# Performance work log

Hardware: AMD Instinct MI355X
Metric: run time of the kernel (lower is better)

The kernel has to match this reference:

```python
import jax, jax.numpy as jnp
import numpy as np

NUM_CLASSES = 80
SCORE_THRESH = 0.5
NMS_THRESH = 0.5
TOP_K = 200  # max candidates kept per (image, class) before greedy NMS


def setup_inputs() -> dict:
    key = jax.random.key(0)
    k1, k2, k3 = jax.random.split(key, 3)
    B, A, HW, C = 8, 3, 5776, NUM_CLASSES  # 608-input YOLOv4 P3 level: 76*76
    # well-formed boxes in [0,1]: x1y1 + positive wh
    xy = jax.random.uniform(k1, (B, A, HW, 2)) * 0.8
    wh = jax.random.uniform(k2, (B, A, HW, 2)) * 0.2 + 0.01
    boxes = jnp.concatenate([xy, xy + wh], axis=-1)
    scores = jax.random.uniform(k3, (B, A, HW, C))
    return {"boxes": boxes, "scores": scores}


def _pairwise_iou(b):
    # b: [K, 4] (x1, y1, x2, y2) -> IoU matrix [K, K] (union mode)
    x1, y1, x2, y2 = b[:, 0], b[:, 1], b[:, 2], b[:, 3]
    area = (x2 - x1) * (y2 - y1)
    xx1 = jnp.maximum(x1[:, None], x1[None, :])
    yy1 = jnp.maximum(y1[:, None], y1[None, :])
    xx2 = jnp.minimum(x2[:, None], x2[None, :])
    yy2 = jnp.minimum(y2[:, None], y2[None, :])
    inter = jnp.maximum(0.0, xx2 - xx1) * jnp.maximum(0.0, yy2 - yy1)
    return inter / (area[:, None] + area[None, :] - inter)


def _nms_one(boxes, scores):
    # boxes: [N, 4], scores: [N] -> top-K candidates with greedy-NMS keep mask
    s = jnp.where(scores > SCORE_THRESH, scores, -jnp.inf)  # score threshold filter
    top_s, idx = jax.lax.top_k(s, TOP_K)                    # descending, like argsort()[::-1]
    b = boxes[idx]                                          # [K, 4]
    valid = jnp.isfinite(top_s)
    iou = _pairwise_iou(b)                                  # [K, K]

    def body(keep, i):
        # if box i survives, suppress all lower-scored boxes with IoU > thresh
        sup = keep[i] & (iou[i] > NMS_THRESH) & (jnp.arange(TOP_K) > i)
        return keep & ~sup, None

    keep, _ = jax.lax.scan(body, valid, jnp.arange(TOP_K))
    return b, top_s, keep


def reference(boxes, scores):
    B, A, HW, _ = boxes.shape
    C = scores.shape[-1]
    b = boxes.reshape(B, A * HW, 4)
    s = scores.reshape(B, A * HW, C)
    per_img = jax.vmap(lambda bb, ss: jax.vmap(_nms_one, in_axes=(None, 1))(bb, ss))
    boxes_k, scores_k, keep = per_img(b, s)  # [B,C,K,4], [B,C,K], [B,C,K]
    cls = jnp.broadcast_to(jnp.arange(C, dtype=boxes.dtype)[None, :, None], keep.shape)
    out_box = jnp.where(keep[..., None], boxes_k, 0.0)
    out_score = jnp.where(keep, scores_k, 0.0)
    out_cls = jnp.where(keep, cls, 0.0)
    # padded detections [B, C, K, 6] = (x1, y1, x2, y2, score, class_id)
    return jnp.concatenate([out_box, out_score[..., None], out_cls[..., None]], axis=-1)
```

## Files before the change

kernel.cpp:

```cpp
#include <hip/hip_runtime.h>
#include <stdint.h>

#define B_IMG  8
#define NANCH  17328
#define NCLS   80
#define TOPK   200
#define NTHR   256
#define NTHRB  512
#define CHUNK  64
#define NCHK   ((NANCH + CHUNK - 1) / CHUNK)
#define NCHKP  272
#define SLOT   24
#define NPOS   (NCHK * SLOT)
#define THRESH_HI 0.9f

__device__ __forceinline__ void hist_add(float s, unsigned int* hist) {
  if (s > 0.5f) {
    unsigned int bin = (__float_as_uint(s) - 0x3F000000u) >> 15;
    if (bin > 255u) bin = 255u;
    atomicAdd(&hist[bin], 1u);
  }
}

__global__ __launch_bounds__(NTHR) void scatter_k(
    const float* __restrict__ scores,
    unsigned char* __restrict__ cnt2,
    unsigned long long* __restrict__ cand) {
  const int nb = blockIdx.x;
  const int b  = blockIdx.y;
  const int tid = threadIdx.x;
  const int wv = tid >> 6, lane = tid & 63;
  const int n0 = nb * CHUNK;

  __shared__ float tile[CHUNK][81];

  const int nrow = (NANCH - n0 < CHUNK) ? (NANCH - n0) : CHUNK;
  const int nf4 = nrow * (NCLS / 4);
  const float4* src4 = (const float4*)(scores + (size_t)(b * NANCH + n0) * NCLS);
  for (int f = tid; f < nf4; f += NTHR) {
    float4 v = src4[f];
    int n = f / 20, c4 = (f - n * 20) * 4;
    tile[n][c4] = v.x; tile[n][c4 + 1] = v.y;
    tile[n][c4 + 2] = v.z; tile[n][c4 + 3] = v.w;
  }
  __syncthreads();

  const bool rv = (lane < nrow);
  const unsigned long long lt = (1ull << lane) - 1ull;
  const int cbase = wv * 20;
#pragma unroll 4
  for (int cc = 0; cc < 20; ++cc) {
    const int c = cbase + cc;
    const int bc = b * NCLS + c;
    float s = rv ? tile[lane][c] : 0.f;
    const bool cd = (s > THRESH_HI);
    unsigned long long bal = __ballot(cd);
    if (cd) {
      unsigned int r = (unsigned int)__popcll(bal & lt);
      if (r < SLOT)
        cand[((size_t)bc * NCHK + nb) * SLOT + r] =
            ((unsigned long long)__float_as_uint(s) << 32) |
            (unsigned long long)(0xFFFFFFFFu - (unsigned int)(n0 + lane));
    }
    if (lane == 0)
      cnt2[(size_t)bc * NCHKP + nb] = (unsigned char)__popcll(bal);
  }
}

__global__ __launch_bounds__(NTHRB) void backend_k(
    const float* __restrict__ scores, const float* __restrict__ boxes,
    const unsigned char* __restrict__ cnt2, const unsigned long long* __restrict__ cand,
    float* __restrict__ out) {
  const int bc = blockIdx.x;
  const int b = bc / NCLS;
  const int c = bc - b * NCLS;
  const int tid = threadIdx.x;
  const int wv = tid >> 6, lane = tid & 63;
  const unsigned long long lt = (1ull << lane) - 1ull;

  __shared__ unsigned long long selk[512];
  __shared__ unsigned long long sorted[256];
  __shared__ unsigned int hist[256];
  __shared__ float sx1[256], sy1[256], sx2[256], sy2[256], sar[256], ssc[256];
  __shared__ int skeep[256];
  __shared__ __align__(16) unsigned long long sup[TOPK][4];
  __shared__ __align__(16) float eout[TOPK * 6];
  __shared__ unsigned int sh_cutbits;
  __shared__ int sh_m, sh_sel, sh_bad;

  if (tid < 256) { hist[tid] = 0u; sorted[tid] = 0ull; }
  if (tid == 0) { sh_m = 0; sh_sel = 0; sh_bad = 0; }
  __syncthreads();

  const unsigned long long* cb0 = cand + (size_t)bc * NCHK * SLOT;
  const unsigned char* ct0 = cnt2 + (size_t)bc * NCHKP;
  for (int p = tid; p < NPOS; p += NTHRB) {
    const int ch = p / SLOT;
    const int sl = p - ch * SLOT;
    unsigned int ci = (unsigned int)ct0[ch];
    if (sl == 0) {
      if (ci > SLOT) sh_bad = 1;
      atomicAdd(&sh_m, (int)ci);
    }
    if (sl < (int)ci && ci <= SLOT) {
      unsigned long long k = cb0[p];
      unsigned int bin = ((unsigned int)(k >> 32) - 0x3F000000u) >> 15;
      if (bin > 255u) bin = 255u;
      atomicAdd(&hist[bin], 1u);
    }
  }
  __syncthreads();

  const bool fb = (sh_bad != 0) || (sh_m < TOPK);

  if (fb) {
    if (tid < 256) hist[tid] = 0u;
    __syncthreads();
    const float* src = scores + (size_t)b * NANCH * NCLS + c;
    for (int i = tid; i < NANCH; i += NTHRB) hist_add(src[(size_t)i * NCLS], hist);
    __syncthreads();
  }

  if (tid < 64) {
    int base = 255 - 4 * tid;
    int s4 = (int)(hist[base] + hist[base - 1] + hist[base - 2] + hist[base - 3]);
    int cum = s4;
    for (int d = 1; d < 64; d <<= 1) {
      int o = __shfl_up(cum, d, 64);
      if (tid >= d) cum += o;
    }
    unsigned long long bal = __ballot(cum >= TOPK);
    if (bal == 0ull) {
      if (tid == 0) sh_cutbits = 0x3F000000u;
    } else {
      int l0 = __builtin_ctzll(bal);
      if (tid == l0) {
        unsigned int acc = (unsigned int)(cum - s4);
        int cutbin = base - 3;
        for (int k = 0; k < 4; ++k) {
          acc += hist[base - k];
          if (acc >= TOPK) { cutbin = base - k; break; }
        }
        sh_cutbits = 0x3F000000u + ((unsigned int)cutbin << 15);
      }
    }
  }
  __syncthreads();
  const unsigned int cutbits = sh_cutbits;

  if (!fb) {
    for (int p = tid; p < NPOS; p += NTHRB) {
      const int ch = p / SLOT;
      const int sl = p - ch * SLOT;
      unsigned int ci = (unsigned int)ct0[ch];
      unsigned long long k = 0ull;
      bool pred = (sl < (int)ci);
      if (pred) k = cb0[p];
      pred = pred && ((unsigned int)(k >> 32) >= cutbits);
      unsigned long long bal = __ballot(pred);
      if (bal) {
        int base0 = 0;
        if (lane == 0) base0 = atomicAdd(&sh_sel, (int)__popcll(bal));
        base0 = __shfl(base0, 0, 64);
        if (pred) {
          int pos = base0 + (int)__popcll(bal & lt);
          if (pos < 512) selk[pos] = k;
        }
      }
    }
  } else {
    const float* src = scores + (size_t)b * NANCH * NCLS + c;
    for (int i = tid; i < NANCH; i += NTHRB) {
      float s = src[(size_t)i * NCLS];
      if (s > 0.5f && __float_as_uint(s) >= cutbits) {
        int slot = atomicAdd(&sh_sel, 1);
        if (slot < 512)
          selk[slot] = ((unsigned long long)__float_as_uint(s) << 32) |
                       (unsigned long long)(0xFFFFFFFFu - (unsigned int)i);
      }
    }
  }
  __syncthreads();

  int Msel = sh_sel; if (Msel > 512) Msel = 512;
  if (tid < Msel) {
    const unsigned long long mk = selk[tid];
    int r = 0;
#pragma unroll 8
    for (int j = 0; j < Msel; ++j) r += (selk[j] > mk) ? 1 : 0;
    if (r < 256) sorted[r] = mk;
  }
  __syncthreads();

  if (tid < 256) {
    unsigned long long key = sorted[tid];
    int valid = (tid < TOPK) && (key != 0ull);
    unsigned int idx = 0xFFFFFFFFu - (unsigned int)(key & 0xFFFFFFFFull);
    float4 bx = make_float4(0.f, 0.f, 0.f, 0.f);
    if (valid) bx = ((const float4*)boxes)[(size_t)b * NANCH + idx];
    sx1[tid] = bx.x; sy1[tid] = bx.y; sx2[tid] = bx.z; sy2[tid] = bx.w;
    sar[tid] = __fmul_rn(bx.z - bx.x, bx.w - bx.y);
    ssc[tid] = valid ? __uint_as_float((unsigned int)(key >> 32)) : 0.f;
    skeep[tid] = valid;
  }
  __syncthreads();

  {
    float jx1[4], jy1[4], jx2[4], jy2[4], ja[4];
#pragma unroll
    for (int r = 0; r < 4; ++r) {
      int j = (r << 6) | lane;
      jx1[r] = sx1[j]; jy1[r] = sy1[j]; jx2[r] = sx2[j]; jy2[r] = sy2[j];
      ja[r] = sar[j];
    }
    for (int i = wv; i < TOPK; i += 8) {
      const float xi1 = sx1[i], yi1 = sy1[i], xi2 = sx2[i], yi2 = sy2[i];
      const float ai = sar[i];
      unsigned long long w[4];
#pragma unroll
      for (int r = 0; r < 4; ++r) {
        unsigned long long word = 0ull;
        if ((r << 6) + 63 > i) {
          const int j = (r << 6) | lane;
          const bool vp = (j > i) && (j < TOPK);
          float xx1 = fmaxf(xi1, jx1[r]);
          float yy1 = fmaxf(yi1, jy1[r]);
          float xx2 = fminf(xi2, jx2[r]);
          float yy2 = fminf(yi2, jy2[r]);
          float iw = fmaxf(0.f, __fsub_rn(xx2, xx1));
          float ih = fmaxf(0.f, __fsub_rn(yy2, yy1));
          float inter = __fmul_rn(iw, ih);
          float denom = __fsub_rn(__fadd_rn(ai, ja[r]), inter);
          float q = __fmul_rn(inter, __builtin_amdgcn_rcpf(denom));
          bool s = vp && (q > 0.5f);
          bool gbad = vp && (fabsf(q - 0.5f) < 1e-5f);
          if (__ballot(gbad)) {
            if (gbad) s = __fdiv_rn(inter, denom) > 0.5f;
          }
          word = __ballot(s);
        }
        w[r] = word;
      }
      if (lane == 0) {
        ulonglong2* dst = (ulonglong2*)&sup[i][0];
        ulonglong2 t0; t0.x = w[0]; t0.y = w[1];
        ulonglong2 t1; t1.x = w[2]; t1.y = w[3];
        dst[0] = t0; dst[1] = t1;
      }
    }
  }
  __syncthreads();

  if (tid < 64) {
    unsigned long long k0 = __ballot(skeep[tid] != 0);
    unsigned long long k1 = __ballot(skeep[64 + tid] != 0);
    unsigned long long k2 = __ballot(skeep[128 + tid] != 0);
    unsigned long long k3 = __ballot(skeep[192 + tid] != 0);
#define NMS_SCAN_WORD(KW, BASE, CNT)                                     \
    _Pragma("unroll 8")                                                  \
    for (int li = 0; li < (CNT); ++li) {                                 \
      const ulonglong2* s2p =                                            \
          reinterpret_cast<const ulonglong2*>(&sup[(BASE) + li][0]);     \
      ulonglong2 sa = s2p[0];                                            \
      ulonglong2 sb = s2p[1];                                            \
      unsigned long long m = 0ull - ((KW >> li) & 1ull);                 \
      k0 &= ~(sa.x & m); k1 &= ~(sa.y & m);                              \
      k2 &= ~(sb.x & m); k3 &= ~(sb.y & m);                              \
    }
    NMS_SCAN_WORD(k0, 0, 64)
    NMS_SCAN_WORD(k1, 64, 64)
    NMS_SCAN_WORD(k2, 128, 64)
    NMS_SCAN_WORD(k3, 192, 8)
#undef NMS_SCAN_WORD
    skeep[tid]        = (int)((k0 >> tid) & 1ull);
    skeep[64 + tid]   = (int)((k1 >> tid) & 1ull);
    skeep[128 + tid]  = (int)((k2 >> tid) & 1ull);
    skeep[192 + tid]  = (int)((k3 >> tid) & 1ull);
  }
  __syncthreads();

  if (tid < TOPK) {
    int kp = skeep[tid];
    eout[tid * 6 + 0] = kp ? sx1[tid] : 0.f;
    eout[tid * 6 + 1] = kp ? sy1[tid] : 0.f;
    eout[tid * 6 + 2] = kp ? sx2[tid] : 0.f;
    eout[tid * 6 + 3] = kp ? sy2[tid] : 0.f;
    eout[tid * 6 + 4] = kp ? ssc[tid] : 0.f;
    eout[tid * 6 + 5] = kp ? (float)c : 0.f;
  }
  __syncthreads();

  float4* out4 = (float4*)(out + (size_t)bc * (TOPK * 6));
  const float4* e4 = (const float4*)eout;
  for (int f = tid; f < (TOPK * 6) / 4; f += NTHRB) out4[f] = e4[f];
}

__global__ __launch_bounds__(NTHR) void select_nms_k(
    const float* __restrict__ boxes, const float* __restrict__ scores,
    float* __restrict__ out) {
  const int blk = blockIdx.x;
  const int b = blk / NCLS;
  const int c = blk - b * NCLS;
  const int tid = threadIdx.x;

  __shared__ unsigned int hist[256];
  __shared__ unsigned long long keys[1024];
  __shared__ float sx1[TOPK], sy1[TOPK], sx2[TOPK], sy2[TOPK], sar[TOPK], ssc[TOPK];
  __shared__ int skeep[TOPK];
  __shared__ unsigned int sh_cutbits;
  __shared__ int sh_m;

  const float* src = scores + (size_t)b * NANCH * NCLS + c;

  for (int j = tid; j < 256; j += NTHR) hist[j] = 0;
  if (tid == 0) sh_m = 0;
  __syncthreads();

  for (int i = tid; i < NANCH; i += NTHR) hist_add(src[(size_t)i * NCLS], hist);
  __syncthreads();

  if (tid == 0) {
    unsigned int acc = 0;
    int cut = 0;
    for (int bin = 255; bin >= 0; --bin) {
      acc += hist[bin];
      if (acc >= TOPK) { cut = bin; break; }
    }
    sh_cutbits = 0x3F000000u + ((unsigned int)cut << 15);
  }
  __syncthreads();
  const unsigned int cutbits = sh_cutbits;

  for (int i = tid; i < NANCH; i += NTHR) {
    float s = src[(size_t)i * NCLS];
    if (s > 0.5f && __float_as_uint(s) >= cutbits) {
      int slot = atomicAdd(&sh_m, 1);
      if (slot < 1024)
        keys[slot] = ((unsigned long long)__float_as_uint(s) << 32) |
                     (unsigned long long)(0xFFFFFFFFu - (unsigned int)i);
    }
  }
  __syncthreads();
  int M = sh_m; if (M > 1024) M = 1024;
  for (int j = M + tid; j < 1024; j += NTHR) keys[j] = 0ull;

  for (int size = 2; size <= 1024; size <<= 1) {
    for (int st = size >> 1; st > 0; st >>= 1) {
      __syncthreads();
      for (int t = tid; t < 512; t += NTHR) {
        int lo = 2 * t - (t & (st - 1));
        int hi = lo + st;
        bool desc = ((lo & size) == 0);
        unsigned long long a = keys[lo], bb = keys[hi];
        if ((a < bb) == desc) { keys[lo] = bb; keys[hi] = a; }
      }
    }
  }
  __syncthreads();

  if (tid < TOPK) {
    unsigned long long key = keys[tid];
    int valid = (key != 0ull);
    float sc = __uint_as_float((unsigned int)(key >> 32));
    unsigned int idx = 0xFFFFFFFFu - (unsigned int)(key & 0xFFFFFFFFull);
    float4 bx = make_float4(0.f, 0.f, 0.f, 0.f);
    if (valid) bx = ((const float4*)boxes)[(size_t)b * NANCH + idx];
    sx1[tid] = bx.x; sy1[tid] = bx.y; sx2[tid] = bx.z; sy2[tid] = bx.w;
    sar[tid] = __fmul_rn(bx.z - bx.x, bx.w - bx.y);
    ssc[tid] = valid ? sc : 0.f;
    skeep[tid] = valid;
  }
  __syncthreads();

  if (tid < 64) {
    const int lane = tid;
    float x1v[4], y1v[4], x2v[4], y2v[4], av[4];
    int km = 0;
#pragma unroll
    for (int r = 0; r < 4; ++r) {
      int j = lane + (r << 6);
      if (j < TOPK) {
        x1v[r] = sx1[j]; y1v[r] = sy1[j]; x2v[r] = sx2[j]; y2v[r] = sy2[j];
        av[r] = sar[j];
        if (skeep[j]) km |= (1 << r);
      } else {
        x1v[r] = 0.f; y1v[r] = 0.f; x2v[r] = 0.f; y2v[r] = 0.f; av[r] = 0.f;
      }
    }
#pragma unroll
    for (int ri = 0; ri < 4; ++ri) {
      const int imax = (ri == 3) ? (TOPK - 192) : 64;
      for (int li = 0; li < imax; ++li) {
        const int i = (ri << 6) + li;
        int kmi = __shfl(km, li, 64);
        if (!((kmi >> ri) & 1)) continue;
        float xi1 = __shfl(x1v[ri], li, 64);
        float yi1 = __shfl(y1v[ri], li, 64);
        float xi2 = __shfl(x2v[ri], li, 64);
        float yi2 = __shfl(y2v[ri], li, 64);
        float ai  = __shfl(av[ri],  li, 64);
#pragma unroll
        for (int r = 0; r < 4; ++r) {
          int j = lane + (r << 6);
          if (j > i && j < TOPK && ((km >> r) & 1)) {
            float xx1 = fmaxf(xi1, x1v[r]);
            float yy1 = fmaxf(yi1, y1v[r]);
            float xx2 = fminf(xi2, x2v[r]);
            float yy2 = fminf(yi2, y2v[r]);
            float iw = fmaxf(0.f, __fsub_rn(xx2, xx1));
            float ih = fmaxf(0.f, __fsub_rn(yy2, yy1));
            float inter = __fmul_rn(iw, ih);
            float denom = __fsub_rn(__fadd_rn(ai, av[r]), inter);
            float iou = __fdiv_rn(inter, denom);
            if (iou > 0.5f) km &= ~(1 << r);
          }
        }
      }
    }
#pragma unroll
    for (int r = 0; r < 4; ++r) {
      int j = lane + (r << 6);
      if (j < TOPK) skeep[j] = (km >> r) & 1;
    }
  }
  __syncthreads();

  const size_t base = ((size_t)b * NCLS + c) * (TOPK * 6);
  for (int f = tid; f < TOPK * 6; f += NTHR) {
    int k = f / 6, comp = f - k * 6;
    float v = 0.f;
    if (skeep[k]) {
      switch (comp) {
        case 0: v = sx1[k]; break;
        case 1: v = sy1[k]; break;
        case 2: v = sx2[k]; break;
        case 3: v = sy2[k]; break;
        case 4: v = ssc[k]; break;
        default: v = (float)c; break;
      }
    }
    out[base + f] = v;
  }
}

extern "C" void kernel_launch(void* const* d_in, const int* in_sizes, int n_in,
                              void* d_out, int out_size, void* d_ws, size_t ws_size,
                              hipStream_t stream) {
  (void)in_sizes; (void)n_in; (void)out_size;
  const float* boxes  = (const float*)d_in[0];
  const float* scores = (const float*)d_in[1];
  float* out = (float*)d_out;

  const int NBC = B_IMG * NCLS;
  const size_t need_c2  = (size_t)NBC * NCHKP;
  const size_t need_cd  = (size_t)NBC * NCHK * SLOT * sizeof(uint64_t);
  const size_t need = need_c2 + need_cd;

  if (ws_size >= need) {
    char* w = (char*)d_ws;
    unsigned char* cnt2      = (unsigned char*)w;       w += need_c2;
    unsigned long long* cand = (unsigned long long*)w;

    scatter_k<<<dim3(NCHK, B_IMG), NTHR, 0, stream>>>(scores, cnt2, cand);
    backend_k<<<NBC, NTHRB, 0, stream>>>(scores, boxes, cnt2, cand, out);
  } else {
    select_nms_k<<<NBC, NTHR, 0, stream>>>(boxes, scores, out);
  }
}
```

Before: 83.00 us.

## Build per-class score histogram in scatter via global atomics, simplify IoU mask

Moves the per-(image,class) score histogram out of the backend kernel and into scatter_k, which accumulates it with global atomics into a zeroed workspace buffer. Overflow chunks are flagged in bin 0. The backend then reads the finished histogram instead of rescanning every candidate slot. The IoU suppression loop is also reworked to apply precomputed bitmasks after the ballots rather than per-lane predicates. This adds an extra init kernel launch and global atomic contention in exchange for removing a full pass over the candidate buffer per block.

```diff
diff --git a/kernel.cpp b/kernel.cpp
--- a/kernel.cpp
+++ b/kernel.cpp
@@ -12,6 +12,7 @@
 #define NCHKP  272
 #define SLOT   24
 #define NPOS   (NCHK * SLOT)
+#define NBC    (B_IMG * NCLS)
 #define THRESH_HI 0.9f
 
 __device__ __forceinline__ void hist_add(float s, unsigned int* hist) {
@@ -22,10 +23,15 @@
   }
 }
 
+__global__ __launch_bounds__(NTHR) void init_gh_k(unsigned int* __restrict__ ghist) {
+  ghist[(size_t)blockIdx.x * NTHR + threadIdx.x] = 0u;
+}
+
 __global__ __launch_bounds__(NTHR) void scatter_k(
     const float* __restrict__ scores,
     unsigned char* __restrict__ cnt2,
-    unsigned long long* __restrict__ cand) {
+    unsigned long long* __restrict__ cand,
+    unsigned int* __restrict__ ghist) {
   const int nb = blockIdx.x;
   const int b  = blockIdx.y;
   const int tid = threadIdx.x;
@@ -61,16 +67,22 @@
         cand[((size_t)bc * NCHK + nb) * SLOT + r] =
             ((unsigned long long)__float_as_uint(s) << 32) |
             (unsigned long long)(0xFFFFFFFFu - (unsigned int)(n0 + lane));
-    }
-    if (lane == 0)
-      cnt2[(size_t)bc * NCHKP + nb] = (unsigned char)__popcll(bal);
+      unsigned int bin = (__float_as_uint(s) - 0x3F000000u) >> 15;
+      if (bin > 255u) bin = 255u;
+      atomicAdd(&ghist[(size_t)bc * 256 + bin], 1u);
+    }
+    if (lane == 0) {
+      unsigned int pc = (unsigned int)__popcll(bal);
+      cnt2[(size_t)bc * NCHKP + nb] = (unsigned char)pc;
+      if (pc > SLOT) atomicAdd(&ghist[(size_t)bc * 256 + 0], 1u);
+    }
   }
 }
 
 __global__ __launch_bounds__(NTHRB) void backend_k(
     const float* __restrict__ scores, const float* __restrict__ boxes,
     const unsigned char* __restrict__ cnt2, const unsigned long long* __restrict__ cand,
-    float* __restrict__ out) {
+    const unsigned int* __restrict__ ghist, float* __restrict__ out) {
   const int bc = blockIdx.x;
   const int b = bc / NCLS;
   const int c = bc - b * NCLS;
@@ -86,40 +98,15 @@
   __shared__ __align__(16) unsigned long long sup[TOPK][4];
   __shared__ __align__(16) float eout[TOPK * 6];
   __shared__ unsigned int sh_cutbits;
-  __shared__ int sh_m, sh_sel, sh_bad;
-
-  if (tid < 256) { hist[tid] = 0u; sorted[tid] = 0ull; }
-  if (tid == 0) { sh_m = 0; sh_sel = 0; sh_bad = 0; }
-  __syncthreads();
-
-  const unsigned long long* cb0 = cand + (size_t)bc * NCHK * SLOT;
-  const unsigned char* ct0 = cnt2 + (size_t)bc * NCHKP;
-  for (int p = tid; p < NPOS; p += NTHRB) {
-    const int ch = p / SLOT;
-    const int sl = p - ch * SLOT;
-    unsigned int ci = (unsigned int)ct0[ch];
-    if (sl == 0) {
-      if (ci > SLOT) sh_bad = 1;
-      atomicAdd(&sh_m, (int)ci);
-    }
-    if (sl < (int)ci && ci <= SLOT) {
-      unsigned long long k = cb0[p];
-      unsigned int bin = ((unsigned int)(k >> 32) - 0x3F000000u) >> 15;
-      if (bin > 255u) bin = 255u;
-      atomicAdd(&hist[bin], 1u);
-    }
-  }
-  __syncthreads();
-
-  const bool fb = (sh_bad != 0) || (sh_m < TOPK);
-
-  if (fb) {
-    if (tid < 256) hist[tid] = 0u;
-    __syncthreads();
-    const float* src = scores + (size_t)b * NANCH * NCLS + c;
-    for (int i = tid; i < NANCH; i += NTHRB) hist_add(src[(size_t)i * NCLS], hist);
-    __syncthreads();
-  }
+  __shared__ int sh_sel, sh_bad, sh_tot;
+
+  if (tid < 256) {
+    unsigned int h = ghist[(size_t)bc * 256 + tid];
+    hist[tid] = h;
+    sorted[tid] = 0ull;
+    if (tid == 0) { sh_sel = 0; sh_bad = (int)h; }
+  }
+  __syncthreads();
 
   if (tid < 64) {
     int base = 255 - 4 * tid;
@@ -129,6 +116,7 @@
       int o = __shfl_up(cum, d, 64);
       if (tid >= d) cum += o;
     }
+    if (tid == 63) sh_tot = cum;
     unsigned long long bal = __ballot(cum >= TOPK);
     if (bal == 0ull) {
       if (tid == 0) sh_cutbits = 0x3F000000u;
@@ -146,9 +134,31 @@
     }
   }
   __syncthreads();
+
+  const bool fb = (sh_bad != 0) || ((sh_tot - sh_bad) < TOPK);
+
+  if (fb) {
+    if (tid < 256) hist[tid] = 0u;
+    __syncthreads();
+    const float* src = scores + (size_t)b * NANCH * NCLS + c;
+    for (int i = tid; i < NANCH; i += NTHRB) hist_add(src[(size_t)i * NCLS], hist);
+    __syncthreads();
+    if (tid == 0) {
+      unsigned int acc = 0;
+      int cut = 0;
+      for (int bin = 255; bin >= 0; --bin) {
+        acc += hist[bin];
+        if (acc >= TOPK) { cut = bin; break; }
+      }
+      sh_cutbits = 0x3F000000u + ((unsigned int)cut << 15);
+    }
+    __syncthreads();
+  }
   const unsigned int cutbits = sh_cutbits;
 
   if (!fb) {
+    const unsigned long long* cb0 = cand + (size_t)bc * NCHK * SLOT;
+    const unsigned char* ct0 = cnt2 + (size_t)bc * NCHKP;
     for (int p = tid; p < NPOS; p += NTHRB) {
       const int ch = p / SLOT;
       const int sl = p - ch * SLOT;
@@ -213,7 +223,13 @@
       jx1[r] = sx1[j]; jy1[r] = sy1[j]; jx2[r] = sx2[j]; jy2[r] = sy2[j];
       ja[r] = sar[j];
     }
-    for (int i = wv; i < TOPK; i += 8) {
+#pragma unroll 2
+    for (int k = 0; k < 25; ++k) {
+      const int i = (k << 3) + wv;
+      const int d = i >> 6;
+      const int il = i & 63;
+      unsigned long long dmask = (il == 63) ? 0ull : ((~0ull) << (il + 1));
+      if (d == 3) dmask &= 0xFFull;
       const float xi1 = sx1[i], yi1 = sy1[i], xi2 = sx2[i], yi2 = sy2[i];
       const float ai = sar[i];
       unsigned long long w[4];
@@ -221,8 +237,8 @@
       for (int r = 0; r < 4; ++r) {
         unsigned long long word = 0ull;
         if ((r << 6) + 63 > i) {
-          const int j = (r << 6) | lane;
-          const bool vp = (j > i) && (j < TOPK);
+          const unsigned long long wmask =
+              (r > d) ? ((r == 3) ? 0xFFull : ~0ull) : dmask;
           float xx1 = fmaxf(xi1, jx1[r]);
           float yy1 = fmaxf(yi1, jy1[r]);
           float xx2 = fminf(xi2, jx2[r]);
@@ -232,12 +248,11 @@
           float inter = __fmul_rn(iw, ih);
           float denom = __fsub_rn(__fadd_rn(ai, ja[r]), inter);
           float q = __fmul_rn(inter, __builtin_amdgcn_rcpf(denom));
-          bool s = vp && (q > 0.5f);
-          bool gbad = vp && (fabsf(q - 0.5f) < 1e-5f);
-          if (__ballot(gbad)) {
-            if (gbad) s = __fdiv_rn(inter, denom) > 0.5f;
-          }
-          word = __ballot(s);
+          word = __ballot(q > 0.5f);
+          unsigned long long gb = __ballot(fabsf(q - 0.5f) < 1e-5f) & wmask;
+          if (gb)
+            word = __ballot(__fdiv_rn(inter, denom) > 0.5f);
+          word &= wmask;
         }
         w[r] = word;
       }
@@ -451,18 +466,20 @@
   const float* scores = (const float*)d_in[1];
   float* out = (float*)d_out;
 
-  const int NBC = B_IMG * NCLS;
   const size_t need_c2  = (size_t)NBC * NCHKP;
   const size_t need_cd  = (size_t)NBC * NCHK * SLOT * sizeof(uint64_t);
-  const size_t need = need_c2 + need_cd;
+  const size_t need_gh  = (size_t)NBC * 256 * sizeof(unsigned int);
+  const size_t need = need_c2 + need_cd + need_gh;
 
   if (ws_size >= need) {
     char* w = (char*)d_ws;
     unsigned char* cnt2      = (unsigned char*)w;       w += need_c2;
-    unsigned long long* cand = (unsigned long long*)w;
-
-    scatter_k<<<dim3(NCHK, B_IMG), NTHR, 0, stream>>>(scores, cnt2, cand);
-    backend_k<<<NBC, NTHRB, 0, stream>>>(scores, boxes, cnt2, cand, out);
+    unsigned long long* cand = (unsigned long long*)w;  w += need_cd;
+    unsigned int* ghist      = (unsigned int*)w;
+
+    init_gh_k<<<NBC, NTHR, 0, stream>>>(ghist);
+    scatter_k<<<dim3(NCHK, B_IMG), NTHR, 0, stream>>>(scores, cnt2, cand, ghist);
+    backend_k<<<NBC, NTHRB, 0, stream>>>(scores, boxes, cnt2, cand, ghist, out);
   } else {
     select_nms_k<<<NBC, NTHR, 0, stream>>>(boxes, scores, out);
   }
```

Result: slower. 102.1 us (+23.0%).
